# Performance work log

Hardware: AMD Instinct MI355X
Metric: run time of the kernel (lower is better)

Reference implementation:

```python
import jax, jax.numpy as jnp
import numpy as np

B, C, H, W = 64, 1, 512, 512
THRESHOLD = 50.0
LEVELS = 3


def _haar_dwt2(x):
    """Single-level 2D Haar DWT on [B,H,W] (even H,W). Returns (cA,(cH,cV,cD)).
    Matches pywt 'haar' coefficient magnitudes (sign conventions are irrelevant
    to the loss, which is odd-symmetric through soft-threshold and uses |.|)."""
    a = x[:, 0::2, 0::2]
    b = x[:, 0::2, 1::2]
    c = x[:, 1::2, 0::2]
    d = x[:, 1::2, 1::2]
    half = jnp.float32(0.5)
    cA = (a + b + c + d) * half
    cH = (a + b - c - d) * half  # low along cols, high along rows
    cV = (a - b + c - d) * half  # high along cols, low along rows
    cD = (a - b - c + d) * half  # high/high
    return cA, (cH, cV, cD)


def _wavedec2(x, levels):
    """Multi-level DWT. Returns detail tuples ordered coarsest-first,
    matching pywt.wavedec2 list order coeffs[1:]."""
    details = []
    cA = x
    for _ in range(levels):
        cA, d = _haar_dwt2(cA)
        details.append(d)
    details.reverse()  # coarsest first
    return details


def _soft_threshold(x, thr):
    return jnp.sign(x) * jnp.maximum(jnp.abs(x) - thr, 0.0)


def setup_inputs() -> dict:
    key = jax.random.key(0)
    k1, k2 = jax.random.split(key)
    pred = jax.random.uniform(k1, (B, C, H, W), dtype=jnp.float32)
    target = jax.random.uniform(k2, (B, C, H, W), dtype=jnp.float32)
    return {"pred": pred, "target": target}


def reference(pred, target):
    p = pred[:, 0]   # [B,H,W]
    t = target[:, 0]
    det_p = _wavedec2(p, LEVELS)
    det_t = _wavedec2(t, LEVELS)
    total = jnp.float32(0.0)
    for level_idx in range(1, LEVELS + 1):
        # per-level adaptive threshold, normalized to [0,1] image range
        thr = jnp.float32((THRESHOLD / 2.0 ** (level_idx - 1)) / 255.0)
        level_weight = jnp.float32(1.0 / level_idx)
        dp = det_p[level_idx - 1]
        dt = det_t[level_idx - 1]
        level_loss = jnp.float32(0.0)
        for k in range(3):  # cH, cV, cD
            diff = _soft_threshold(dp[k], thr) - _soft_threshold(dt[k], thr)
            level_loss = level_loss + jnp.mean(jnp.abs(diff))
        total = total + level_weight * level_loss / 3.0
    # per-sample sum / valid_samples == batch mean (all samples valid here)
    return total
```

## Files before the change

### kernel.cpp

```cpp
#include <hip/hip_runtime.h>


#define IMG_W 512
#define N_BATCH 64

#define THR1 (50.0f / 255.0f)
#define THR2 (25.0f / 255.0f)
#define THR3 (12.5f / 255.0f)

#define NBLK 2048

typedef float v4f __attribute__((ext_vector_type(4)));

__device__ __forceinline__ float softthr(float x, float thr) {
    float m = fmaxf(fabsf(x) - thr, 0.0f);
    return copysignf(m, x);
}

__device__ __forceinline__ float detail_term(float p, float t, float thr) {
    return fabsf(softthr(p, thr) - softthr(t, thr));
}

__device__ __forceinline__ void haar_quad(float a, float b, float c, float d,
                                          float& cA, float& cH, float& cV, float& cD) {
    cA = 0.5f * (a + b + c + d);
    cH = 0.5f * (a + b - c - d);
    cV = 0.5f * (a - b + c - d);
    cD = 0.5f * (a - b - c + d);
}

__device__ __forceinline__ v4f ld4nt(const float* p) {
    return __builtin_nontemporal_load((const v4f*)p);
}

__global__ __launch_bounds__(256, 4)
void wavelet_main(const float* __restrict__ pred,
                  const float* __restrict__ target,
                  float* __restrict__ ws) {
    constexpr float W1 = 1.0f / (1.0f * 3.0f * (float)(N_BATCH * 256 * 256));
    constexpr float W2 = 1.0f / (2.0f * 3.0f * (float)(N_BATCH * 128 * 128));
    constexpr float W3 = 1.0f / (3.0f * 3.0f * (float)(N_BATCH * 64 * 64));

    const int T  = blockIdx.x * 4 + (threadIdx.x >> 6);
    const int li = threadIdx.x & 63;

    const int img   = T >> 7;
    const int rem   = T & 127;
    const int half  = rem & 1;
    const int strip = rem >> 1;

    const size_t off = (size_t)img * (512 * 512)
                     + (size_t)strip * 8 * IMG_W
                     + half * 256 + 4 * li;
    const float* pb = pred + off;
    const float* tb = target + off;

    v4f P0 = ld4nt(pb);                 v4f P1 = ld4nt(pb + IMG_W);
    v4f P2 = ld4nt(pb + 2 * IMG_W);     v4f P3 = ld4nt(pb + 3 * IMG_W);
    v4f P4 = ld4nt(pb + 4 * IMG_W);     v4f P5 = ld4nt(pb + 5 * IMG_W);
    v4f P6 = ld4nt(pb + 6 * IMG_W);     v4f P7 = ld4nt(pb + 7 * IMG_W);
    v4f Q0 = ld4nt(tb);                 v4f Q1 = ld4nt(tb + IMG_W);
    v4f Q2 = ld4nt(tb + 2 * IMG_W);     v4f Q3 = ld4nt(tb + 3 * IMG_W);
    v4f Q4 = ld4nt(tb + 4 * IMG_W);     v4f Q5 = ld4nt(tb + 5 * IMG_W);
    v4f Q6 = ld4nt(tb + 6 * IMG_W);     v4f Q7 = ld4nt(tb + 7 * IMG_W);

    float s1 = 0.0f, s2 = 0.0f;
    float cA1p[4][2], cA1t[4][2];

    {
        float cA, cH, cV, cD, cAt, cHt, cVt, cDt;

        #define L1_PAIR(a, b, qa, qb, rp)                                              \
        {                                                                              \
            haar_quad((a).x, (a).y, (b).x, (b).y, cA, cH, cV, cD);                     \
            haar_quad((qa).x, (qa).y, (qb).x, (qb).y, cAt, cHt, cVt, cDt);             \
            s1 += detail_term(cH, cHt, THR1) + detail_term(cV, cVt, THR1)              \
                + detail_term(cD, cDt, THR1);                                          \
            cA1p[rp][0] = cA; cA1t[rp][0] = cAt;                                       \
            haar_quad((a).z, (a).w, (b).z, (b).w, cA, cH, cV, cD);                     \
            haar_quad((qa).z, (qa).w, (qb).z, (qb).w, cAt, cHt, cVt, cDt);             \
            s1 += detail_term(cH, cHt, THR1) + detail_term(cV, cVt, THR1)              \
                + detail_term(cD, cDt, THR1);                                          \
            cA1p[rp][1] = cA; cA1t[rp][1] = cAt;                                       \
        }

        L1_PAIR(P0, P1, Q0, Q1, 0)
        L1_PAIR(P2, P3, Q2, Q3, 1)
        L1_PAIR(P4, P5, Q4, Q5, 2)
        L1_PAIR(P6, P7, Q6, Q7, 3)
        #undef L1_PAIR
    }

    float cA2p[2], cA2t[2];
    {
        float cH, cV, cD, cHt, cVt, cDt;
        haar_quad(cA1p[0][0], cA1p[0][1], cA1p[1][0], cA1p[1][1], cA2p[0], cH, cV, cD);
        haar_quad(cA1t[0][0], cA1t[0][1], cA1t[1][0], cA1t[1][1], cA2t[0], cHt, cVt, cDt);
        s2 += detail_term(cH, cHt, THR2) + detail_term(cV, cVt, THR2) + detail_term(cD, cDt, THR2);
        haar_quad(cA1p[2][0], cA1p[2][1], cA1p[3][0], cA1p[3][1], cA2p[1], cH, cV, cD);
        haar_quad(cA1t[2][0], cA1t[2][1], cA1t[3][0], cA1t[3][1], cA2t[1], cHt, cVt, cDt);
        s2 += detail_term(cH, cHt, THR2) + detail_term(cV, cVt, THR2) + detail_term(cD, cDt, THR2);
    }

    float s3;
    {
        const float bP = __shfl_xor(cA2p[0], 1);
        const float dP = __shfl_xor(cA2p[1], 1);
        const float bT = __shfl_xor(cA2t[0], 1);
        const float dT = __shfl_xor(cA2t[1], 1);
        float cA, cH, cV, cD, cAt, cHt, cVt, cDt;
        haar_quad(cA2p[0], bP, cA2p[1], dP, cA, cH, cV, cD);
        haar_quad(cA2t[0], bT, cA2t[1], dT, cAt, cHt, cVt, cDt);
        s3 = detail_term(cH, cHt, THR3) + detail_term(cV, cVt, THR3) + detail_term(cD, cDt, THR3);
    }
    const float w3 = (li & 1) ? 0.0f : W3;

    float acc = W1 * s1 + W2 * s2 + w3 * s3;

    #pragma unroll
    for (int off = 32; off > 0; off >>= 1)
        acc += __shfl_down(acc, off, 64);

    __shared__ float wave_sums[4];
    const int lane_b = threadIdx.x & 63;
    const int wave_b = threadIdx.x >> 6;
    if (lane_b == 0) wave_sums[wave_b] = acc;
    __syncthreads();
    if (threadIdx.x == 0)
        ws[blockIdx.x] = wave_sums[0] + wave_sums[1] + wave_sums[2] + wave_sums[3];
}

__global__ __launch_bounds__(256)
void wavelet_reduce(const float* __restrict__ ws, float* __restrict__ out) {
    const int tidx = threadIdx.x;
    float v = 0.0f;
    #pragma unroll
    for (int k = 0; k < NBLK / 256; ++k)
        v += ws[tidx + k * 256];

    #pragma unroll
    for (int off = 32; off > 0; off >>= 1)
        v += __shfl_down(v, off, 64);

    __shared__ float wave_sums[4];
    const int lane = tidx & 63;
    const int wave = tidx >> 6;
    if (lane == 0) wave_sums[wave] = v;
    __syncthreads();
    if (tidx == 0)
        out[0] = wave_sums[0] + wave_sums[1] + wave_sums[2] + wave_sums[3];
}

extern "C" void kernel_launch(void* const* d_in, const int* in_sizes, int n_in,
                              void* d_out, int out_size, void* d_ws, size_t ws_size,
                              hipStream_t stream) {
    const float* pred   = (const float*)d_in[0];
    const float* target = (const float*)d_in[1];
    float* out = (float*)d_out;
    float* ws  = (float*)d_ws;

    wavelet_main<<<NBLK, 256, 0, stream>>>(pred, target, ws);
    wavelet_reduce<<<1, 256, 0, stream>>>(ws, out);
}
```

Measured before the change: 137.0 us.

## Process two tiles per wave with software-pipelined loads overlapping compute

Halves the grid so each wave handles two 8-row tiles. Loads for the second tile are issued in two halves, interleaved with the Haar computation of the first tile, so memory latency overlaps with ALU work. The intent is to hide load latency and amortise per-block reduction overhead. The cost is fewer waves in flight and higher register pressure, which can lower occupancy on a purely memory-bound kernel.

```diff
diff --git a/kernel.cpp b/kernel.cpp
--- a/kernel.cpp
+++ b/kernel.cpp
@@ -8,7 +8,8 @@
 #define THR2 (25.0f / 255.0f)
 #define THR3 (12.5f / 255.0f)
 
-#define NBLK 2048
+#define NBLK   1024
+#define NWAVES 4096
 
 typedef float v4f __attribute__((ext_vector_type(4)));
 
@@ -33,89 +34,115 @@
     return __builtin_nontemporal_load((const v4f*)p);
 }
 
+__device__ __forceinline__ size_t tile_offset(int T, int li) {
+    const int img   = T >> 7;
+    const int rem   = T & 127;
+    const int half  = rem & 1;
+    const int strip = rem >> 1;
+    return (size_t)img * (512 * 512)
+         + (size_t)strip * 8 * IMG_W
+         + half * 256 + 4 * li;
+}
+
+__device__ __forceinline__ void half_A(v4f P0, v4f P1, v4f P2, v4f P3,
+                                       v4f Q0, v4f Q1, v4f Q2, v4f Q3,
+                                       float& s1, float& s2,
+                                       float& cA2p0, float& cA2t0) {
+    float cA, cH, cV, cD, cAt, cHt, cVt, cDt;
+    float p00, p01, p10, p11, t00, t01, t10, t11;
+
+    haar_quad(P0.x, P0.y, P1.x, P1.y, cA, cH, cV, cD);
+    haar_quad(Q0.x, Q0.y, Q1.x, Q1.y, cAt, cHt, cVt, cDt);
+    s1 += detail_term(cH, cHt, THR1) + detail_term(cV, cVt, THR1) + detail_term(cD, cDt, THR1);
+    p00 = cA; t00 = cAt;
+    haar_quad(P0.z, P0.w, P1.z, P1.w, cA, cH, cV, cD);
+    haar_quad(Q0.z, Q0.w, Q1.z, Q1.w, cAt, cHt, cVt, cDt);
+    s1 += detail_term(cH, cHt, THR1) + detail_term(cV, cVt, THR1) + detail_term(cD, cDt, THR1);
+    p01 = cA; t01 = cAt;
+
+    haar_quad(P2.x, P2.y, P3.x, P3.y, cA, cH, cV, cD);
+    haar_quad(Q2.x, Q2.y, Q3.x, Q3.y, cAt, cHt, cVt, cDt);
+    s1 += detail_term(cH, cHt, THR1) + detail_term(cV, cVt, THR1) + detail_term(cD, cDt, THR1);
+    p10 = cA; t10 = cAt;
+    haar_quad(P2.z, P2.w, P3.z, P3.w, cA, cH, cV, cD);
+    haar_quad(Q2.z, Q2.w, Q3.z, Q3.w, cAt, cHt, cVt, cDt);
+    s1 += detail_term(cH, cHt, THR1) + detail_term(cV, cVt, THR1) + detail_term(cD, cDt, THR1);
+    p11 = cA; t11 = cAt;
+
+    haar_quad(p00, p01, p10, p11, cA2p0, cH, cV, cD);
+    haar_quad(t00, t01, t10, t11, cA2t0, cHt, cVt, cDt);
+    s2 += detail_term(cH, cHt, THR2) + detail_term(cV, cVt, THR2) + detail_term(cD, cDt, THR2);
+}
+
+__device__ __forceinline__ float tile_finish(float s1, float s2,
+                                             float cA2p0, float cA2p1,
+                                             float cA2t0, float cA2t1,
+                                             float w3m) {
+    constexpr float W1 = 1.0f / (1.0f * 3.0f * (float)(N_BATCH * 256 * 256));
+    constexpr float W2 = 1.0f / (2.0f * 3.0f * (float)(N_BATCH * 128 * 128));
+    constexpr float W3 = 1.0f / (3.0f * 3.0f * (float)(N_BATCH * 64 * 64));
+
+    const float bP = __shfl_xor(cA2p0, 1);
+    const float dP = __shfl_xor(cA2p1, 1);
+    const float bT = __shfl_xor(cA2t0, 1);
+    const float dT = __shfl_xor(cA2t1, 1);
+    float cA, cH, cV, cD, cAt, cHt, cVt, cDt;
+    haar_quad(cA2p0, bP, cA2p1, dP, cA, cH, cV, cD);
+    haar_quad(cA2t0, bT, cA2t1, dT, cAt, cHt, cVt, cDt);
+    const float s3 = detail_term(cH, cHt, THR3) + detail_term(cV, cVt, THR3)
+                   + detail_term(cD, cDt, THR3);
+    return W1 * s1 + W2 * s2 + (w3m * W3) * s3;
+}
+
 __global__ __launch_bounds__(256, 4)
 void wavelet_main(const float* __restrict__ pred,
                   const float* __restrict__ target,
                   float* __restrict__ ws) {
-    constexpr float W1 = 1.0f / (1.0f * 3.0f * (float)(N_BATCH * 256 * 256));
-    constexpr float W2 = 1.0f / (2.0f * 3.0f * (float)(N_BATCH * 128 * 128));
-    constexpr float W3 = 1.0f / (3.0f * 3.0f * (float)(N_BATCH * 64 * 64));
+    const int wid = blockIdx.x * 4 + (threadIdx.x >> 6);
+    const int li  = threadIdx.x & 63;
 
-    const int T  = blockIdx.x * 4 + (threadIdx.x >> 6);
-    const int li = threadIdx.x & 63;
+    const size_t off0 = tile_offset(wid, li);
+    const size_t off1 = tile_offset(wid + NWAVES, li);
+    const float* pb0 = pred + off0;
+    const float* tb0 = target + off0;
+    const float* pb1 = pred + off1;
+    const float* tb1 = target + off1;
 
-    const int img   = T >> 7;
-    const int rem   = T & 127;
-    const int half  = rem & 1;
-    const int strip = rem >> 1;
+    const float w3m = (li & 1) ? 0.0f : 1.0f;
+    float acc = 0.0f;
 
-    const size_t off = (size_t)img * (512 * 512)
-                     + (size_t)strip * 8 * IMG_W
-                     + half * 256 + 4 * li;
-    const float* pb = pred + off;
-    const float* tb = target + off;
-
-    v4f P0 = ld4nt(pb);                 v4f P1 = ld4nt(pb + IMG_W);
-    v4f P2 = ld4nt(pb + 2 * IMG_W);     v4f P3 = ld4nt(pb + 3 * IMG_W);
-    v4f P4 = ld4nt(pb + 4 * IMG_W);     v4f P5 = ld4nt(pb + 5 * IMG_W);
-    v4f P6 = ld4nt(pb + 6 * IMG_W);     v4f P7 = ld4nt(pb + 7 * IMG_W);
-    v4f Q0 = ld4nt(tb);                 v4f Q1 = ld4nt(tb + IMG_W);
-    v4f Q2 = ld4nt(tb + 2 * IMG_W);     v4f Q3 = ld4nt(tb + 3 * IMG_W);
-    v4f Q4 = ld4nt(tb + 4 * IMG_W);     v4f Q5 = ld4nt(tb + 5 * IMG_W);
-    v4f Q6 = ld4nt(tb + 6 * IMG_W);     v4f Q7 = ld4nt(tb + 7 * IMG_W);
+    v4f A0 = ld4nt(pb0);             v4f A1 = ld4nt(pb0 + IMG_W);
+    v4f A2 = ld4nt(pb0 + 2 * IMG_W); v4f A3 = ld4nt(pb0 + 3 * IMG_W);
+    v4f QA0 = ld4nt(tb0);             v4f QA1 = ld4nt(tb0 + IMG_W);
+    v4f QA2 = ld4nt(tb0 + 2 * IMG_W); v4f QA3 = ld4nt(tb0 + 3 * IMG_W);
+    v4f B0 = ld4nt(pb0 + 4 * IMG_W); v4f B1 = ld4nt(pb0 + 5 * IMG_W);
+    v4f B2 = ld4nt(pb0 + 6 * IMG_W); v4f B3 = ld4nt(pb0 + 7 * IMG_W);
+    v4f QB0 = ld4nt(tb0 + 4 * IMG_W); v4f QB1 = ld4nt(tb0 + 5 * IMG_W);
+    v4f QB2 = ld4nt(tb0 + 6 * IMG_W); v4f QB3 = ld4nt(tb0 + 7 * IMG_W);
 
     float s1 = 0.0f, s2 = 0.0f;
-    float cA1p[4][2], cA1t[4][2];
+    float cA2p0, cA2t0, cA2p1, cA2t1;
 
-    {
-        float cA, cH, cV, cD, cAt, cHt, cVt, cDt;
+    half_A(A0, A1, A2, A3, QA0, QA1, QA2, QA3, s1, s2, cA2p0, cA2t0);
 
-        #define L1_PAIR(a, b, qa, qb, rp)                                              \
-        {                                                                              \
-            haar_quad((a).x, (a).y, (b).x, (b).y, cA, cH, cV, cD);                     \
-            haar_quad((qa).x, (qa).y, (qb).x, (qb).y, cAt, cHt, cVt, cDt);             \
-            s1 += detail_term(cH, cHt, THR1) + detail_term(cV, cVt, THR1)              \
-                + detail_term(cD, cDt, THR1);                                          \
-            cA1p[rp][0] = cA; cA1t[rp][0] = cAt;                                       \
-            haar_quad((a).z, (a).w, (b).z, (b).w, cA, cH, cV, cD);                     \
-            haar_quad((qa).z, (qa).w, (qb).z, (qb).w, cAt, cHt, cVt, cDt);             \
-            s1 += detail_term(cH, cHt, THR1) + detail_term(cV, cVt, THR1)              \
-                + detail_term(cD, cDt, THR1);                                          \
-            cA1p[rp][1] = cA; cA1t[rp][1] = cAt;                                       \
-        }
+    A0 = ld4nt(pb1);             A1 = ld4nt(pb1 + IMG_W);
+    A2 = ld4nt(pb1 + 2 * IMG_W); A3 = ld4nt(pb1 + 3 * IMG_W);
+    QA0 = ld4nt(tb1);             QA1 = ld4nt(tb1 + IMG_W);
+    QA2 = ld4nt(tb1 + 2 * IMG_W); QA3 = ld4nt(tb1 + 3 * IMG_W);
 
-        L1_PAIR(P0, P1, Q0, Q1, 0)
-        L1_PAIR(P2, P3, Q2, Q3, 1)
-        L1_PAIR(P4, P5, Q4, Q5, 2)
-        L1_PAIR(P6, P7, Q6, Q7, 3)
-        #undef L1_PAIR
-    }
+    half_A(B0, B1, B2, B3, QB0, QB1, QB2, QB3, s1, s2, cA2p1, cA2t1);
 
-    float cA2p[2], cA2t[2];
-    {
-        float cH, cV, cD, cHt, cVt, cDt;
-        haar_quad(cA1p[0][0], cA1p[0][1], cA1p[1][0], cA1p[1][1], cA2p[0], cH, cV, cD);
-        haar_quad(cA1t[0][0], cA1t[0][1], cA1t[1][0], cA1t[1][1], cA2t[0], cHt, cVt, cDt);
-        s2 += detail_term(cH, cHt, THR2) + detail_term(cV, cVt, THR2) + detail_term(cD, cDt, THR2);
-        haar_quad(cA1p[2][0], cA1p[2][1], cA1p[3][0], cA1p[3][1], cA2p[1], cH, cV, cD);
-        haar_quad(cA1t[2][0], cA1t[2][1], cA1t[3][0], cA1t[3][1], cA2t[1], cHt, cVt, cDt);
-        s2 += detail_term(cH, cHt, THR2) + detail_term(cV, cVt, THR2) + detail_term(cD, cDt, THR2);
-    }
+    acc += tile_finish(s1, s2, cA2p0, cA2p1, cA2t0, cA2t1, w3m);
 
-    float s3;
-    {
-        const float bP = __shfl_xor(cA2p[0], 1);
-        const float dP = __shfl_xor(cA2p[1], 1);
-        const float bT = __shfl_xor(cA2t[0], 1);
-        const float dT = __shfl_xor(cA2t[1], 1);
-        float cA, cH, cV, cD, cAt, cHt, cVt, cDt;
-        haar_quad(cA2p[0], bP, cA2p[1], dP, cA, cH, cV, cD);
-        haar_quad(cA2t[0], bT, cA2t[1], dT, cAt, cHt, cVt, cDt);
-        s3 = detail_term(cH, cHt, THR3) + detail_term(cV, cVt, THR3) + detail_term(cD, cDt, THR3);
-    }
-    const float w3 = (li & 1) ? 0.0f : W3;
+    B0 = ld4nt(pb1 + 4 * IMG_W); B1 = ld4nt(pb1 + 5 * IMG_W);
+    B2 = ld4nt(pb1 + 6 * IMG_W); B3 = ld4nt(pb1 + 7 * IMG_W);
+    QB0 = ld4nt(tb1 + 4 * IMG_W); QB1 = ld4nt(tb1 + 5 * IMG_W);
+    QB2 = ld4nt(tb1 + 6 * IMG_W); QB3 = ld4nt(tb1 + 7 * IMG_W);
 
-    float acc = W1 * s1 + W2 * s2 + w3 * s3;
+    s1 = 0.0f; s2 = 0.0f;
+    half_A(A0, A1, A2, A3, QA0, QA1, QA2, QA3, s1, s2, cA2p0, cA2t0);
+    half_A(B0, B1, B2, B3, QB0, QB1, QB2, QB3, s1, s2, cA2p1, cA2t1);
+    acc += tile_finish(s1, s2, cA2p0, cA2p1, cA2t0, cA2t1, w3m);
 
     #pragma unroll
     for (int off = 32; off > 0; off >>= 1)
```

Result: no change. 135.5 us, median of 2 (-1.1%).
